# Kernel optimization log

Measured on AMD Instinct MI355X. Metric: run time of the kernel, lower is better.

## Reference

```python
import jax, jax.numpy as jnp
import numpy as np

N_NODES = 100000
N_EDGES = 1600000
IN_DIM, HID_DIM, OUT_DIM = 2, 128, 128


def setup_inputs() -> dict:
    key = jax.random.key(0)
    ks = jax.random.split(key, 8)
    x = jax.random.normal(ks[0], (N_NODES, IN_DIM), dtype=jnp.float32)
    edge_index = jax.random.randint(ks[1], (2, N_EDGES), 0, N_NODES, dtype=jnp.int64)
    s = 0.1
    return {
        "x": x,
        "edge_index": edge_index,
        # SAGEConv layer 1: lin_l (on aggregated neighbors, with bias) + lin_r (root)
        "W_l1": jax.random.normal(ks[2], (IN_DIM, HID_DIM), dtype=jnp.float32) * s,
        "W_r1": jax.random.normal(ks[3], (IN_DIM, HID_DIM), dtype=jnp.float32) * s,
        "b1": jnp.zeros((HID_DIM,), dtype=jnp.float32),
        # SAGEConv layer 2
        "W_l2": jax.random.normal(ks[4], (HID_DIM, OUT_DIM), dtype=jnp.float32) * s,
        "W_r2": jax.random.normal(ks[5], (HID_DIM, OUT_DIM), dtype=jnp.float32) * s,
        "b2": jnp.zeros((OUT_DIM,), dtype=jnp.float32),
    }


def _sage_conv(h, src, dst, Wl, Wr, b):
    # PyG SAGEConv (aggr='mean'): out_i = Wl @ mean_{j in N(i)} h_j + Wr @ h_i + b
    msg = h[src]                                              # [E, D] gather
    agg = jax.ops.segment_sum(msg, dst, num_segments=N_NODES)  # [N, D] scatter-add
    deg = jax.ops.segment_sum(jnp.ones_like(dst, dtype=h.dtype), dst,
                              num_segments=N_NODES)
    agg = agg / jnp.maximum(deg, 1.0)[:, None]                # mean aggregation
    return agg @ Wl + h @ Wr + b


def reference(x, edge_index, W_l1, W_r1, b1, W_l2, W_r2, b2):
    src, dst = edge_index[0], edge_index[1]  # messages flow src -> dst
    h = _sage_conv(x, src, dst, W_l1, W_r1, b1)
    h = jax.nn.relu(h)  # dropout p=0.1 is identity in eval mode
    out = _sage_conv(h, src, dst, W_l2, W_r2, b2)
    return out
```

## Files before the change

kernel.cpp:

```cpp
#include <hip/hip_runtime.h>


using f32x4 = __attribute__((ext_vector_type(4))) float;
using f32x2 = __attribute__((ext_vector_type(2))) float;
using s16x8 = __attribute__((ext_vector_type(8))) short;

__device__ __forceinline__ unsigned short f32_to_bf16(float f) {
  unsigned int u = __float_as_uint(f);
  u += 0x7fffu + ((u >> 16) & 1u);
  return (unsigned short)(u >> 16);
}

#define EDGE_TILE 4096

__global__ __launch_bounds__(256) void k_bhist(const int* __restrict__ ei, int* __restrict__ bcnt,
                                               int E, int nb) {
  __shared__ int h[1024];
  int t = threadIdx.x;
  for (int i = t; i < nb; i += 256) h[i] = 0;
  __syncthreads();
  int tbeg = blockIdx.x * EDGE_TILE;
  int tend = min(tbeg + EDGE_TILE, E);
  const int* dstp = ei + E;
  for (int i = tbeg + t; i < tend; i += 256) atomicAdd(&h[dstp[i] >> 7], 1);
  __syncthreads();
  for (int i = t; i < nb; i += 256) if (h[i]) atomicAdd(&bcnt[i], h[i]);
}

__global__ __launch_bounds__(1024) void k_bscan(const int* __restrict__ bcnt, int* __restrict__ bbase,
                                                int* __restrict__ bcur, int nb, int E) {
  __shared__ int sm[2][1024];
  int t = threadIdx.x;
  int v0 = (t < nb) ? bcnt[t] : 0;
  sm[0][t] = v0;
  __syncthreads();
  int src = 0;
  for (int st = 1; st < 1024; st <<= 1) {
    int v = sm[src][t];
    if (t >= st) v += sm[src][t - st];
    sm[src ^ 1][t] = v; __syncthreads(); src ^= 1;
  }
  int ex = sm[src][t] - v0;
  if (t < nb) { bbase[t] = ex; bcur[t] = ex; }
  if (t == 0) bbase[nb] = E;
}

__global__ __launch_bounds__(256) void k_bscatter(const int* __restrict__ ei, int* __restrict__ bcur,
                                                  unsigned int* __restrict__ ebuf, int E, int nb) {
  __shared__ int h[1024];
  __shared__ int base[1024];
  int t = threadIdx.x;
  for (int i = t; i < nb; i += 256) h[i] = 0;
  __syncthreads();
  int tbeg = blockIdx.x * EDGE_TILE;
  int tend = min(tbeg + EDGE_TILE, E);
  const int* srcp = ei;
  const int* dstp = ei + E;
  for (int i = tbeg + t; i < tend; i += 256) atomicAdd(&h[dstp[i] >> 7], 1);
  __syncthreads();
  for (int i = t; i < nb; i += 256) {
    int c = h[i];
    base[i] = c ? atomicAdd(&bcur[i], c) : 0;
    h[i] = 0;
  }
  __syncthreads();
  for (int i = tbeg + t; i < tend; i += 256) {
    int d = dstp[i];
    int b = d >> 7;
    int r = atomicAdd(&h[b], 1);
    ebuf[base[b] + r] = ((unsigned)srcp[i] << 7) | (unsigned)(d & 127);
  }
}

__global__ __launch_bounds__(256) void k_bucket_csr(const unsigned int* __restrict__ ebuf,
                                                    const int* __restrict__ bbase,
                                                    const float* __restrict__ x,
                                                    int* __restrict__ offs, int* __restrict__ csr,
                                                    float* __restrict__ agg1,
                                                    int N, int nb) {
  __shared__ int deg[128];
  __shared__ int loff[128];
  __shared__ int cur[128];
  __shared__ float sx0[128];
  __shared__ float sx1[128];
  int b = blockIdx.x;
  int t = threadIdx.x;
  int lo = bbase[b], hi = bbase[b + 1];
  if (t < 128) { deg[t] = 0; sx0[t] = 0.f; sx1[t] = 0.f; }
  __syncthreads();
  const float2* x2 = (const float2*)x;
  for (int i = lo + t; i < hi; i += 256) {
    unsigned int e = ebuf[i];
    int d = e & 127;
    float2 v = x2[e >> 7];
    atomicAdd(&deg[d], 1);
    atomicAdd(&sx0[d], v.x);
    atomicAdd(&sx1[d], v.y);
  }
  __syncthreads();
  if (t < 128) loff[t] = deg[t];
  __syncthreads();
  for (int st = 1; st < 128; st <<= 1) {
    int v = 0;
    if (t < 128 && t >= st) v = loff[t - st];
    __syncthreads();
    if (t < 128) loff[t] += v;
    __syncthreads();
  }
  if (t < 128) {
    int ex = loff[t] - deg[t];
    cur[t] = ex;
    int node = b * 128 + t;
    if (node < N) {
      offs[node] = lo + ex;
      agg1[2 * node]     = sx0[t];
      agg1[2 * node + 1] = sx1[t];
    }
  }
  if (b == nb - 1 && t == 0) offs[N] = hi;
  __syncthreads();
  for (int i = lo + t; i < hi; i += 256) {
    unsigned int e = ebuf[i];
    int r = atomicAdd(&cur[e & 127], 1);
    csr[lo + r] = (int)(e >> 7);
  }
}

__global__ __launch_bounds__(256) void k_layer1(const float* __restrict__ x, const float* __restrict__ agg1,
                                                const int* __restrict__ offs,
                                                const float* __restrict__ Wl, const float* __restrict__ Wr,
                                                const float* __restrict__ b1,
                                                unsigned int* __restrict__ h16,
                                                unsigned short* __restrict__ h8, int n) {
  int gid = blockIdx.x * 256 + threadIdx.x;
  int node = gid >> 6;
  if (node >= n) return;
  int c = (gid & 63) * 2;
  int deg = offs[node + 1] - offs[node];
  float sc = 1.0f / (float)max(deg, 1);
  float a0 = agg1[2 * node] * sc, a1 = agg1[2 * node + 1] * sc;
  float x0 = x[2 * node], x1 = x[2 * node + 1];
  float r0 = fmaf(a0, Wl[c],     fmaf(a1, Wl[128 + c],     fmaf(x0, Wr[c],     fmaf(x1, Wr[128 + c],     b1[c]))));
  float r1 = fmaf(a0, Wl[c + 1], fmaf(a1, Wl[128 + c + 1], fmaf(x0, Wr[c + 1], fmaf(x1, Wr[128 + c + 1], b1[c + 1]))));
  r0 = r0 > 0.f ? r0 : 0.f;
  r1 = r1 > 0.f ? r1 : 0.f;
  unsigned int packed = (unsigned int)f32_to_bf16(r0) | ((unsigned int)f32_to_bf16(r1) << 16);
  h16[(size_t)node * 64 + (gid & 63)] = packed;
  unsigned int p8 = (unsigned int)__builtin_amdgcn_cvt_pk_fp8_f32(r0, r1, 0, false);
  h8[(size_t)node * 64 + (gid & 63)] = (unsigned short)(p8 & 0xffffu);
}

__global__ __launch_bounds__(256) void k_prepw(const float* __restrict__ Wl2, const float* __restrict__ Wr2,
                                               unsigned short* __restrict__ wt) {
  int tid = blockIdx.x * 256 + threadIdx.x;
  if (tid >= 128 * 256) return;
  int c = tid >> 8, k = tid & 255;
  float v = (k < 128) ? Wl2[k * 128 + c] : Wr2[(k - 128) * 128 + c];
  wt[tid] = f32_to_bf16(v);
}

#define ACC8(v)                                                                              \
  do {                                                                                       \
    f32x2 p;                                                                                 \
    p = __builtin_amdgcn_cvt_pk_f32_fp8((int)(v).x, false); acc[0] += p[0];  acc[1] += p[1]; \
    p = __builtin_amdgcn_cvt_pk_f32_fp8((int)(v).x, true);  acc[2] += p[0];  acc[3] += p[1]; \
    p = __builtin_amdgcn_cvt_pk_f32_fp8((int)(v).y, false); acc[4] += p[0];  acc[5] += p[1]; \
    p = __builtin_amdgcn_cvt_pk_f32_fp8((int)(v).y, true);  acc[6] += p[0];  acc[7] += p[1]; \
    p = __builtin_amdgcn_cvt_pk_f32_fp8((int)(v).z, false); acc[8] += p[0];  acc[9] += p[1]; \
    p = __builtin_amdgcn_cvt_pk_f32_fp8((int)(v).z, true);  acc[10] += p[0]; acc[11] += p[1];\
    p = __builtin_amdgcn_cvt_pk_f32_fp8((int)(v).w, false); acc[12] += p[0]; acc[13] += p[1];\
    p = __builtin_amdgcn_cvt_pk_f32_fp8((int)(v).w, true);  acc[14] += p[0]; acc[15] += p[1];\
  } while (0)

__global__ __launch_bounds__(256) void k_agg2(const int* __restrict__ offs, const int* __restrict__ csr,
                                              const unsigned char* __restrict__ h8,
                                              unsigned int* __restrict__ a16, int n) {
  int wv   = threadIdx.x >> 6;
  int lane = threadIdx.x & 63;
  int sub  = lane >> 3;
  int cb   = lane & 7;
  int node = blockIdx.x * 32 + wv * 8 + sub;
  if (node >= n) return;
  int beg = offs[node];
  int end = offs[node + 1];
  int deg = end - beg;
  const unsigned char* hb = h8 + cb * 16;

  float acc[16];
#pragma unroll
  for (int j = 0; j < 16; ++j) acc[j] = 0.f;

  int t = 0;
  for (; t + 1 < deg; t += 2) {
    int s0 = csr[beg + t];
    int s1 = csr[beg + t + 1];
    uint4 v0 = *(const uint4*)(hb + (size_t)s0 * 128);
    uint4 v1 = *(const uint4*)(hb + (size_t)s1 * 128);
    ACC8(v0);
    ACC8(v1);
  }
  if (t < deg) {
    int s0 = csr[beg + t];
    uint4 v0 = *(const uint4*)(hb + (size_t)s0 * 128);
    ACC8(v0);
  }

  float scale = 1.0f / (float)max(deg, 1);
  unsigned int u[8];
#pragma unroll
  for (int k = 0; k < 8; ++k)
    u[k] = (unsigned int)f32_to_bf16(acc[2 * k] * scale) |
           ((unsigned int)f32_to_bf16(acc[2 * k + 1] * scale) << 16);
  unsigned int* dst = a16 + (size_t)node * 64 + cb * 8;
  *(uint4*)dst       = make_uint4(u[0], u[1], u[2], u[3]);
  *(uint4*)(dst + 4) = make_uint4(u[4], u[5], u[6], u[7]);
}

__global__ __launch_bounds__(256) void k_gemm(const unsigned short* __restrict__ a16,
                                              const unsigned short* __restrict__ h16,
                                              const unsigned short* __restrict__ wt,
                                              const float* __restrict__ b2,
                                              float* __restrict__ out, int nrows) {
  __shared__ unsigned short bs[64 * 264];
  int half = blockIdx.x & 1;
  int tg   = blockIdx.x >> 1;

#pragma unroll
  for (int i = 0; i < 8; ++i) {
    int c = threadIdx.x + i * 256;
    int row = c >> 5, off = c & 31;
    *(uint4*)(bs + row * 264 + off * 8) =
        *(const uint4*)(wt + ((size_t)(half * 64 + row)) * 256 + off * 8);
  }
  __syncthreads();

  int wv   = threadIdx.x >> 6;
  int lane = threadIdx.x & 63;
  int m16 = lane & 15, quad = lane >> 4;
  int tile = tg * 4 + wv;
  if (tile * 16 >= nrows) return;

  int r  = tile * 16 + m16;
  int rc = r < nrows ? r : nrows - 1;
  const unsigned short* arow = a16 + (size_t)rc * 128 + quad * 8;
  const unsigned short* hrow = h16 + (size_t)rc * 128 + quad * 8;

  s16x8 afrag[8];
#pragma unroll
  for (int c4 = 0; c4 < 4; ++c4) {
    afrag[c4]     = *(const s16x8*)(arow + c4 * 32);
    afrag[4 + c4] = *(const s16x8*)(hrow + c4 * 32);
  }

  f32x4 acc[4];
#pragma unroll
  for (int t = 0; t < 4; ++t) acc[t] = (f32x4){0.f, 0.f, 0.f, 0.f};

  const unsigned short* bbase = bs + m16 * 264 + quad * 8;
#pragma unroll
  for (int ch = 0; ch < 8; ++ch) {
#pragma unroll
    for (int t = 0; t < 4; ++t) {
      s16x8 bf = *(const s16x8*)(bbase + t * 16 * 264 + ch * 32);
      acc[t] = __builtin_amdgcn_mfma_f32_16x16x32_bf16(afrag[ch], bf, acc[t], 0, 0, 0);
    }
  }

#pragma unroll
  for (int t = 0; t < 4; ++t) {
    int col = half * 64 + t * 16 + m16;
    float bias = b2[col];
#pragma unroll
    for (int i = 0; i < 4; ++i) {
      int row = tile * 16 + quad * 4 + i;
      if (row < nrows) out[(size_t)row * 128 + col] = acc[t][i] + bias;
    }
  }
}

extern "C" void kernel_launch(void* const* d_in, const int* in_sizes, int n_in,
                              void* d_out, int out_size, void* d_ws, size_t ws_size,
                              hipStream_t stream) {
  const float* x    = (const float*)d_in[0];
  const int*   ei   = (const int*)d_in[1];
  const float* Wl1  = (const float*)d_in[2];
  const float* Wr1  = (const float*)d_in[3];
  const float* b1   = (const float*)d_in[4];
  const float* Wl2  = (const float*)d_in[5];
  const float* Wr2  = (const float*)d_in[6];
  const float* b2   = (const float*)d_in[7];
  float* out = (float*)d_out;

  const int N = in_sizes[0] / 2;
  const int E = in_sizes[1] / 2;
  const int nb = (N + 127) >> 7;

  char* p = (char*)d_ws;
  auto take = [&](size_t bytes) { char* r = p; p += (bytes + 255) & ~(size_t)255; return r; };
  int* bcnt            = (int*)take(1024 * 4);
  int* bbase           = (int*)take(1025 * 4);
  int* bcur            = (int*)take(1024 * 4);
  int* offs            = (int*)take((size_t)(N + 1) * 4);
  int* csr             = (int*)take((size_t)E * 4);
  unsigned int* ebuf   = (unsigned int*)take((size_t)E * 4);
  float* agg1          = (float*)take((size_t)N * 2 * 4);
  unsigned short* h16  = (unsigned short*)take((size_t)N * 128 * 2);
  unsigned short* a16  = (unsigned short*)take((size_t)N * 128 * 2);
  unsigned short* h8   = (unsigned short*)take((size_t)N * 128);
  unsigned short* wt   = (unsigned short*)take((size_t)128 * 256 * 2);

  const int nblk_e = (E + EDGE_TILE - 1) / EDGE_TILE;
  const int ntiles = (N + 15) / 16;

  hipMemsetAsync(bcnt, 0, 1024 * 4, stream);

  k_bhist     <<<nblk_e, 256, 0, stream>>>(ei, bcnt, E, nb);
  k_bscan     <<<1, 1024, 0, stream>>>(bcnt, bbase, bcur, nb, E);
  k_bscatter  <<<nblk_e, 256, 0, stream>>>(ei, bcur, ebuf, E, nb);
  k_bucket_csr<<<nb, 256, 0, stream>>>(ebuf, bbase, x, offs, csr, agg1, N, nb);
  k_layer1    <<<((size_t)N * 64 + 255) / 256, 256, 0, stream>>>(x, agg1, offs, Wl1, Wr1, b1,
                                                                 (unsigned int*)h16, h8, N);
  k_prepw     <<<(128 * 256) / 256, 256, 0, stream>>>(Wl2, Wr2, wt);
  k_agg2      <<<(N + 31) / 32, 256, 0, stream>>>(offs, csr, (const unsigned char*)h8,
                                                  (unsigned int*)a16, N);
  k_gemm      <<<((ntiles + 3) / 4) * 2, 256, 0, stream>>>(a16, h16, wt, b2, out, N);
}
```

Before: 250.7 us.

## Replace bucketed CSR build with global-atomic degree histogram, scan and scatter

Builds the CSR directly with per-node global atomics: a degree histogram, a single-block chunked scan producing offsets, and an atomic scatter of sources. Layer-1 aggregation moves into k_layer1, where one wavefront per node gathers neighbor features via the CSR. This removes the bucket scatter and bucket-local CSR passes and the intermediate edge buffer. The trade-off is heavy random global atomics and scattered writes, a serial per-thread scan over all nodes in one block, and nondeterministic neighbor order.

```diff
diff --git a/kernel.cpp b/kernel.cpp
--- a/kernel.cpp
+++ b/kernel.cpp
@@ -11,143 +11,111 @@
   return (unsigned short)(u >> 16);
 }
 
-#define EDGE_TILE 4096
-
-__global__ __launch_bounds__(256) void k_bhist(const int* __restrict__ ei, int* __restrict__ bcnt,
-                                               int E, int nb) {
-  __shared__ int h[1024];
-  int t = threadIdx.x;
-  for (int i = t; i < nb; i += 256) h[i] = 0;
-  __syncthreads();
-  int tbeg = blockIdx.x * EDGE_TILE;
-  int tend = min(tbeg + EDGE_TILE, E);
+__global__ __launch_bounds__(256) void k_deghist(const int* __restrict__ ei,
+                                                 int* __restrict__ deg, int E) {
   const int* dstp = ei + E;
-  for (int i = tbeg + t; i < tend; i += 256) atomicAdd(&h[dstp[i] >> 7], 1);
-  __syncthreads();
-  for (int i = t; i < nb; i += 256) if (h[i]) atomicAdd(&bcnt[i], h[i]);
-}
-
-__global__ __launch_bounds__(1024) void k_bscan(const int* __restrict__ bcnt, int* __restrict__ bbase,
-                                                int* __restrict__ bcur, int nb, int E) {
+  int stride = gridDim.x * 256;
+  int half = E >> 1;
+  for (int i = blockIdx.x * 256 + threadIdx.x; i < half; i += stride) {
+    int2 d = ((const int2*)dstp)[i];
+    atomicAdd(&deg[d.x], 1);
+    atomicAdd(&deg[d.y], 1);
+  }
+  if ((E & 1) && blockIdx.x == 0 && threadIdx.x == 0)
+    atomicAdd(&deg[dstp[E - 1]], 1);
+}
+
+__global__ __launch_bounds__(1024) void k_scan(const int* __restrict__ deg,
+                                               int* __restrict__ offs,
+                                               int* __restrict__ cur, int N, int E) {
   __shared__ int sm[2][1024];
   int t = threadIdx.x;
-  int v0 = (t < nb) ? bcnt[t] : 0;
-  sm[0][t] = v0;
+  int chunk = (N + 1023) >> 10;
+  int lo = min(t * chunk, N), hi = min(lo + chunk, N);
+  int s = 0;
+  for (int i = lo; i < hi; ++i) s += deg[i];
+  sm[0][t] = s;
   __syncthreads();
   int src = 0;
   for (int st = 1; st < 1024; st <<= 1) {
     int v = sm[src][t];
     if (t >= st) v += sm[src][t - st];
-    sm[src ^ 1][t] = v; __syncthreads(); src ^= 1;
-  }
-  int ex = sm[src][t] - v0;
-  if (t < nb) { bbase[t] = ex; bcur[t] = ex; }
-  if (t == 0) bbase[nb] = E;
-}
-
-__global__ __launch_bounds__(256) void k_bscatter(const int* __restrict__ ei, int* __restrict__ bcur,
-                                                  unsigned int* __restrict__ ebuf, int E, int nb) {
-  __shared__ int h[1024];
-  __shared__ int base[1024];
-  int t = threadIdx.x;
-  for (int i = t; i < nb; i += 256) h[i] = 0;
-  __syncthreads();
-  int tbeg = blockIdx.x * EDGE_TILE;
-  int tend = min(tbeg + EDGE_TILE, E);
+    sm[src ^ 1][t] = v;
+    __syncthreads();
+    src ^= 1;
+  }
+  int base = sm[src][t] - s;
+  for (int i = lo; i < hi; ++i) {
+    int d = deg[i];
+    offs[i] = base;
+    cur[i] = base;
+    base += d;
+  }
+  if (t == 1023) offs[N] = E;
+}
+
+__global__ __launch_bounds__(256) void k_scatter(const int* __restrict__ ei,
+                                                 int* __restrict__ cur,
+                                                 int* __restrict__ csr, int E) {
   const int* srcp = ei;
   const int* dstp = ei + E;
-  for (int i = tbeg + t; i < tend; i += 256) atomicAdd(&h[dstp[i] >> 7], 1);
-  __syncthreads();
-  for (int i = t; i < nb; i += 256) {
-    int c = h[i];
-    base[i] = c ? atomicAdd(&bcur[i], c) : 0;
-    h[i] = 0;
-  }
-  __syncthreads();
-  for (int i = tbeg + t; i < tend; i += 256) {
-    int d = dstp[i];
-    int b = d >> 7;
-    int r = atomicAdd(&h[b], 1);
-    ebuf[base[b] + r] = ((unsigned)srcp[i] << 7) | (unsigned)(d & 127);
-  }
-}
-
-__global__ __launch_bounds__(256) void k_bucket_csr(const unsigned int* __restrict__ ebuf,
-                                                    const int* __restrict__ bbase,
-                                                    const float* __restrict__ x,
-                                                    int* __restrict__ offs, int* __restrict__ csr,
-                                                    float* __restrict__ agg1,
-                                                    int N, int nb) {
-  __shared__ int deg[128];
-  __shared__ int loff[128];
-  __shared__ int cur[128];
-  __shared__ float sx0[128];
-  __shared__ float sx1[128];
-  int b = blockIdx.x;
-  int t = threadIdx.x;
-  int lo = bbase[b], hi = bbase[b + 1];
-  if (t < 128) { deg[t] = 0; sx0[t] = 0.f; sx1[t] = 0.f; }
-  __syncthreads();
-  const float2* x2 = (const float2*)x;
-  for (int i = lo + t; i < hi; i += 256) {
-    unsigned int e = ebuf[i];
-    int d = e & 127;
-    float2 v = x2[e >> 7];
-    atomicAdd(&deg[d], 1);
-    atomicAdd(&sx0[d], v.x);
-    atomicAdd(&sx1[d], v.y);
-  }
-  __syncthreads();
-  if (t < 128) loff[t] = deg[t];
-  __syncthreads();
-  for (int st = 1; st < 128; st <<= 1) {
-    int v = 0;
-    if (t < 128 && t >= st) v = loff[t - st];
-    __syncthreads();
-    if (t < 128) loff[t] += v;
-    __syncthreads();
-  }
-  if (t < 128) {
-    int ex = loff[t] - deg[t];
-    cur[t] = ex;
-    int node = b * 128 + t;
-    if (node < N) {
-      offs[node] = lo + ex;
-      agg1[2 * node]     = sx0[t];
-      agg1[2 * node + 1] = sx1[t];
-    }
-  }
-  if (b == nb - 1 && t == 0) offs[N] = hi;
-  __syncthreads();
-  for (int i = lo + t; i < hi; i += 256) {
-    unsigned int e = ebuf[i];
-    int r = atomicAdd(&cur[e & 127], 1);
-    csr[lo + r] = (int)(e >> 7);
-  }
-}
-
-__global__ __launch_bounds__(256) void k_layer1(const float* __restrict__ x, const float* __restrict__ agg1,
+  int stride = gridDim.x * 256;
+  int half = E >> 1;
+  for (int i = blockIdx.x * 256 + threadIdx.x; i < half; i += stride) {
+    int2 s = ((const int2*)srcp)[i];
+    int2 d = ((const int2*)dstp)[i];
+    int r0 = atomicAdd(&cur[d.x], 1);
+    csr[r0] = s.x;
+    int r1 = atomicAdd(&cur[d.y], 1);
+    csr[r1] = s.y;
+  }
+  if ((E & 1) && blockIdx.x == 0 && threadIdx.x == 0) {
+    int r = atomicAdd(&cur[dstp[E - 1]], 1);
+    csr[r] = srcp[E - 1];
+  }
+}
+
+__global__ __launch_bounds__(256) void k_layer1(const float* __restrict__ x,
                                                 const int* __restrict__ offs,
-                                                const float* __restrict__ Wl, const float* __restrict__ Wr,
+                                                const int* __restrict__ csr,
+                                                const float* __restrict__ Wl,
+                                                const float* __restrict__ Wr,
                                                 const float* __restrict__ b1,
                                                 unsigned int* __restrict__ h16,
                                                 unsigned short* __restrict__ h8, int n) {
-  int gid = blockIdx.x * 256 + threadIdx.x;
-  int node = gid >> 6;
+  int wv = threadIdx.x >> 6;
+  int lane = threadIdx.x & 63;
+  int node = blockIdx.x * 4 + wv;
   if (node >= n) return;
-  int c = (gid & 63) * 2;
-  int deg = offs[node + 1] - offs[node];
+  int beg = offs[node];
+  int end = offs[node + 1];
+  int deg = end - beg;
+  const float2* x2 = (const float2*)x;
+
+  float ax = 0.f, ay = 0.f;
+  for (int t = lane; t < deg; t += 64) {
+    float2 v = x2[csr[beg + t]];
+    ax += v.x;
+    ay += v.y;
+  }
+#pragma unroll
+  for (int off = 32; off; off >>= 1) {
+    ax += __shfl_xor(ax, off);
+    ay += __shfl_xor(ay, off);
+  }
   float sc = 1.0f / (float)max(deg, 1);
-  float a0 = agg1[2 * node] * sc, a1 = agg1[2 * node + 1] * sc;
-  float x0 = x[2 * node], x1 = x[2 * node + 1];
-  float r0 = fmaf(a0, Wl[c],     fmaf(a1, Wl[128 + c],     fmaf(x0, Wr[c],     fmaf(x1, Wr[128 + c],     b1[c]))));
-  float r1 = fmaf(a0, Wl[c + 1], fmaf(a1, Wl[128 + c + 1], fmaf(x0, Wr[c + 1], fmaf(x1, Wr[128 + c + 1], b1[c + 1]))));
+  float a0 = ax * sc, a1 = ay * sc;
+  float2 xv = x2[node];
+
+  int c = lane * 2;
+  float r0 = fmaf(a0, Wl[c],     fmaf(a1, Wl[128 + c],     fmaf(xv.x, Wr[c],     fmaf(xv.y, Wr[128 + c],     b1[c]))));
+  float r1 = fmaf(a0, Wl[c + 1], fmaf(a1, Wl[128 + c + 1], fmaf(xv.x, Wr[c + 1], fmaf(xv.y, Wr[128 + c + 1], b1[c + 1]))));
   r0 = r0 > 0.f ? r0 : 0.f;
   r1 = r1 > 0.f ? r1 : 0.f;
   unsigned int packed = (unsigned int)f32_to_bf16(r0) | ((unsigned int)f32_to_bf16(r1) << 16);
-  h16[(size_t)node * 64 + (gid & 63)] = packed;
+  h16[(size_t)node * 64 + lane] = packed;
   unsigned int p8 = (unsigned int)__builtin_amdgcn_cvt_pk_fp8_f32(r0, r1, 0, false);
-  h8[(size_t)node * 64 + (gid & 63)] = (unsigned short)(p8 & 0xffffu);
+  h8[(size_t)node * 64 + lane] = (unsigned short)(p8 & 0xffffu);
 }
 
 __global__ __launch_bounds__(256) void k_prepw(const float* __restrict__ Wl2, const float* __restrict__ Wr2,
@@ -293,35 +261,29 @@
 
   const int N = in_sizes[0] / 2;
   const int E = in_sizes[1] / 2;
-  const int nb = (N + 127) >> 7;
 
   char* p = (char*)d_ws;
   auto take = [&](size_t bytes) { char* r = p; p += (bytes + 255) & ~(size_t)255; return r; };
-  int* bcnt            = (int*)take(1024 * 4);
-  int* bbase           = (int*)take(1025 * 4);
-  int* bcur            = (int*)take(1024 * 4);
+  int* deg             = (int*)take((size_t)N * 4);
   int* offs            = (int*)take((size_t)(N + 1) * 4);
+  int* cur             = (int*)take((size_t)N * 4);
   int* csr             = (int*)take((size_t)E * 4);
-  unsigned int* ebuf   = (unsigned int*)take((size_t)E * 4);
-  float* agg1          = (float*)take((size_t)N * 2 * 4);
   unsigned short* h16  = (unsigned short*)take((size_t)N * 128 * 2);
   unsigned short* a16  = (unsigned short*)take((size_t)N * 128 * 2);
   unsigned short* h8   = (unsigned short*)take((size_t)N * 128);
   unsigned short* wt   = (unsigned short*)take((size_t)128 * 256 * 2);
 
-  const int nblk_e = (E + EDGE_TILE - 1) / EDGE_TILE;
   const int ntiles = (N + 15) / 16;
 
-  hipMemsetAsync(bcnt, 0, 1024 * 4, stream);
-
-  k_bhist     <<<nblk_e, 256, 0, stream>>>(ei, bcnt, E, nb);
-  k_bscan     <<<1, 1024, 0, stream>>>(bcnt, bbase, bcur, nb, E);
-  k_bscatter  <<<nblk_e, 256, 0, stream>>>(ei, bcur, ebuf, E, nb);
-  k_bucket_csr<<<nb, 256, 0, stream>>>(ebuf, bbase, x, offs, csr, agg1, N, nb);
-  k_layer1    <<<((size_t)N * 64 + 255) / 256, 256, 0, stream>>>(x, agg1, offs, Wl1, Wr1, b1,
-                                                                 (unsigned int*)h16, h8, N);
-  k_prepw     <<<(128 * 256) / 256, 256, 0, stream>>>(Wl2, Wr2, wt);
-  k_agg2      <<<(N + 31) / 32, 256, 0, stream>>>(offs, csr, (const unsigned char*)h8,
-                                                  (unsigned int*)a16, N);
-  k_gemm      <<<((ntiles + 3) / 4) * 2, 256, 0, stream>>>(a16, h16, wt, b2, out, N);
-}
+  hipMemsetAsync(deg, 0, (size_t)N * 4, stream);
+
+  k_deghist <<<2048, 256, 0, stream>>>(ei, deg, E);
+  k_scan    <<<1, 1024, 0, stream>>>(deg, offs, cur, N, E);
+  k_scatter <<<2048, 256, 0, stream>>>(ei, cur, csr, E);
+  k_layer1  <<<(N + 3) / 4, 256, 0, stream>>>(x, offs, csr, Wl1, Wr1, b1,
+                                              (unsigned int*)h16, h8, N);
+  k_prepw   <<<(128 * 256) / 256, 256, 0, stream>>>(Wl2, Wr2, wt);
+  k_agg2    <<<(N + 31) / 32, 256, 0, stream>>>(offs, csr, (const unsigned char*)h8,
+                                                (unsigned int*)a16, N);
+  k_gemm    <<<((ntiles + 3) / 4) * 2, 256, 0, stream>>>(a16, h16, wt, b2, out, N);
+}
```

New measurement: 595.5 us. 2.38x slower.

## Replace scatter-pass atomic bucket reservation with per-tile histograms and column prefix

Applied to the files above, without the earlier changes.

The histogram kernel now stores each edge tile's per-bucket counts. A new column-prefix kernel turns them into per-tile offsets, so the scatter kernel no longer rebuilds the histogram or reserves slots with global atomics. This removes a second pass over dst and the atomic contention on bucket cursors, and makes the bucket layout deterministic. In exchange it adds an extra launch and a serial loop over about 391 tiles per bucket thread, running on only 4 blocks. Separately, the layer-2 aggregation loop is unrolled to issue four neighbor gathers at a time instead of two.

```diff
diff --git a/kernel.cpp b/kernel.cpp
--- a/kernel.cpp
+++ b/kernel.cpp
@@ -14,7 +14,7 @@
 #define EDGE_TILE 4096
 
 __global__ __launch_bounds__(256) void k_bhist(const int* __restrict__ ei, int* __restrict__ bcnt,
-                                               int E, int nb) {
+                                               unsigned short* __restrict__ hcnt, int E, int nb) {
   __shared__ int h[1024];
   int t = threadIdx.x;
   for (int i = t; i < nb; i += 256) h[i] = 0;
@@ -24,11 +24,16 @@
   const int* dstp = ei + E;
   for (int i = tbeg + t; i < tend; i += 256) atomicAdd(&h[dstp[i] >> 7], 1);
   __syncthreads();
-  for (int i = t; i < nb; i += 256) if (h[i]) atomicAdd(&bcnt[i], h[i]);
+  unsigned short* hr = hcnt + (size_t)blockIdx.x * nb;
+  for (int i = t; i < nb; i += 256) {
+    int c = h[i];
+    hr[i] = (unsigned short)c;
+    if (c) atomicAdd(&bcnt[i], c);
+  }
 }
 
 __global__ __launch_bounds__(1024) void k_bscan(const int* __restrict__ bcnt, int* __restrict__ bbase,
-                                                int* __restrict__ bcur, int nb, int E) {
+                                                int nb, int E) {
   __shared__ int sm[2][1024];
   int t = threadIdx.x;
   int v0 = (t < nb) ? bcnt[t] : 0;
@@ -40,30 +45,41 @@
     if (t >= st) v += sm[src][t - st];
     sm[src ^ 1][t] = v; __syncthreads(); src ^= 1;
   }
-  int ex = sm[src][t] - v0;
-  if (t < nb) { bbase[t] = ex; bcur[t] = ex; }
+  if (t < nb) bbase[t] = sm[src][t] - v0;
   if (t == 0) bbase[nb] = E;
 }
 
-__global__ __launch_bounds__(256) void k_bscatter(const int* __restrict__ ei, int* __restrict__ bcur,
+__global__ __launch_bounds__(256) void k_colpre(const unsigned short* __restrict__ hcnt,
+                                                unsigned short* __restrict__ rel,
+                                                int nblk, int nb) {
+  int b = blockIdx.x * 256 + threadIdx.x;
+  if (b >= nb) return;
+  int run = 0;
+  for (int t = 0; t < nblk; ++t) {
+    size_t idx = (size_t)t * nb + b;
+    int c = hcnt[idx];
+    rel[idx] = (unsigned short)run;
+    run += c;
+  }
+}
+
+__global__ __launch_bounds__(256) void k_bscatter(const int* __restrict__ ei,
+                                                  const int* __restrict__ bbase,
+                                                  const unsigned short* __restrict__ rel,
                                                   unsigned int* __restrict__ ebuf, int E, int nb) {
   __shared__ int h[1024];
   __shared__ int base[1024];
   int t = threadIdx.x;
-  for (int i = t; i < nb; i += 256) h[i] = 0;
+  const unsigned short* rr = rel + (size_t)blockIdx.x * nb;
+  for (int i = t; i < nb; i += 256) {
+    h[i] = 0;
+    base[i] = bbase[i] + (int)rr[i];
+  }
   __syncthreads();
   int tbeg = blockIdx.x * EDGE_TILE;
   int tend = min(tbeg + EDGE_TILE, E);
   const int* srcp = ei;
   const int* dstp = ei + E;
-  for (int i = tbeg + t; i < tend; i += 256) atomicAdd(&h[dstp[i] >> 7], 1);
-  __syncthreads();
-  for (int i = t; i < nb; i += 256) {
-    int c = h[i];
-    base[i] = c ? atomicAdd(&bcur[i], c) : 0;
-    h[i] = 0;
-  }
-  __syncthreads();
   for (int i = tbeg + t; i < tend; i += 256) {
     int d = dstp[i];
     int b = d >> 7;
@@ -191,15 +207,21 @@
   for (int j = 0; j < 16; ++j) acc[j] = 0.f;
 
   int t = 0;
-  for (; t + 1 < deg; t += 2) {
+  for (; t + 3 < deg; t += 4) {
     int s0 = csr[beg + t];
     int s1 = csr[beg + t + 1];
+    int s2 = csr[beg + t + 2];
+    int s3 = csr[beg + t + 3];
     uint4 v0 = *(const uint4*)(hb + (size_t)s0 * 128);
     uint4 v1 = *(const uint4*)(hb + (size_t)s1 * 128);
+    uint4 v2 = *(const uint4*)(hb + (size_t)s2 * 128);
+    uint4 v3 = *(const uint4*)(hb + (size_t)s3 * 128);
     ACC8(v0);
     ACC8(v1);
-  }
-  if (t < deg) {
+    ACC8(v2);
+    ACC8(v3);
+  }
+  for (; t < deg; ++t) {
     int s0 = csr[beg + t];
     uint4 v0 = *(const uint4*)(hb + (size_t)s0 * 128);
     ACC8(v0);
@@ -294,12 +316,14 @@
   const int N = in_sizes[0] / 2;
   const int E = in_sizes[1] / 2;
   const int nb = (N + 127) >> 7;
+  const int nblk_e = (E + EDGE_TILE - 1) / EDGE_TILE;
 
   char* p = (char*)d_ws;
   auto take = [&](size_t bytes) { char* r = p; p += (bytes + 255) & ~(size_t)255; return r; };
   int* bcnt            = (int*)take(1024 * 4);
   int* bbase           = (int*)take(1025 * 4);
-  int* bcur            = (int*)take(1024 * 4);
+  unsigned short* hcnt = (unsigned short*)take((size_t)nblk_e * nb * 2);
+  unsigned short* rel  = (unsigned short*)take((size_t)nblk_e * nb * 2);
   int* offs            = (int*)take((size_t)(N + 1) * 4);
   int* csr             = (int*)take((size_t)E * 4);
   unsigned int* ebuf   = (unsigned int*)take((size_t)E * 4);
@@ -309,14 +333,14 @@
   unsigned short* h8   = (unsigned short*)take((size_t)N * 128);
   unsigned short* wt   = (unsigned short*)take((size_t)128 * 256 * 2);
 
-  const int nblk_e = (E + EDGE_TILE - 1) / EDGE_TILE;
   const int ntiles = (N + 15) / 16;
 
   hipMemsetAsync(bcnt, 0, 1024 * 4, stream);
 
-  k_bhist     <<<nblk_e, 256, 0, stream>>>(ei, bcnt, E, nb);
-  k_bscan     <<<1, 1024, 0, stream>>>(bcnt, bbase, bcur, nb, E);
-  k_bscatter  <<<nblk_e, 256, 0, stream>>>(ei, bcur, ebuf, E, nb);
+  k_bhist     <<<nblk_e, 256, 0, stream>>>(ei, bcnt, hcnt, E, nb);
+  k_bscan     <<<1, 1024, 0, stream>>>(bcnt, bbase, nb, E);
+  k_colpre    <<<(nb + 255) / 256, 256, 0, stream>>>(hcnt, rel, nblk_e, nb);
+  k_bscatter  <<<nblk_e, 256, 0, stream>>>(ei, bbase, rel, ebuf, E, nb);
   k_bucket_csr<<<nb, 256, 0, stream>>>(ebuf, bbase, x, offs, csr, agg1, N, nb);
   k_layer1    <<<((size_t)N * 64 + 255) / 256, 256, 0, stream>>>(x, agg1, offs, Wl1, Wr1, b1,
                                                                  (unsigned int*)h16, h8, N);
```

Measured after the change: 349.1 us. 1.39x slower.
